# Performance work log

Hardware: AMD Instinct MI355X
Metric: run time of the kernel (lower is better)

Reference implementation:

```python
import jax, jax.numpy as jnp
import numpy as np

N_NODES = 245760      # 8192 graphs * 30 atoms
N_GRAPHS = 8192
N_EDGES = 1000000
NODES_PER_GRAPH = 30
F_NODE = 78
F_CELL = 1000
HID = 64


def _lin(key, fan_in, fan_out):
    kw, kb = jax.random.split(key)
    s = 1.0 / np.sqrt(fan_in)
    W = jax.random.uniform(kw, (fan_in, fan_out), minval=-s, maxval=s, dtype=jnp.float32)
    b = jax.random.uniform(kb, (fan_out,), minval=-s, maxval=s, dtype=jnp.float32)
    return W, b


def setup_inputs() -> dict:
    key = jax.random.key(0)
    ks = jax.random.split(key, 14)
    x = jax.random.normal(ks[0], (N_NODES, F_NODE), dtype=jnp.float32)
    # edges constrained within each graph: node = graph_id * 30 + local offset
    offs = jax.random.randint(ks[1], (2, N_EDGES), 0, NODES_PER_GRAPH)
    ge = jax.random.randint(ks[2], (N_EDGES,), 0, N_GRAPHS)
    edge_index = (ge[None, :] * NODES_PER_GRAPH + offs).astype(jnp.int64)
    batch = jnp.repeat(jnp.arange(N_GRAPHS, dtype=jnp.int64), NODES_PER_GRAPH)
    cell_features = jax.random.normal(ks[3], (N_GRAPHS, F_CELL), dtype=jnp.float32)
    W1, b1 = _lin(ks[4], F_NODE, HID)
    W2, b2 = _lin(ks[5], HID, 2 * HID)
    W3, b3 = _lin(ks[6], 2 * HID, 4 * HID)
    Wd, bd = _lin(ks[7], 4 * HID, HID)          # drug_embed_fc
    Wc1, bc1 = _lin(ks[8], F_CELL, 2 * HID)      # cell_fc1
    Wc2, bc2 = _lin(ks[9], 2 * HID, HID)         # cell_fc2
    Wm1, bm1 = _lin(ks[10], 2 * HID, HID)        # combiner_fc1
    Wm2, bm2 = _lin(ks[11], HID, 32)             # combiner_fc2
    Wo, bo = _lin(ks[12], 32, 1)                 # output_fc
    return {"x": x, "edge_index": edge_index, "batch": batch,
            "cell_features": cell_features,
            "W1": W1, "b1": b1, "W2": W2, "b2": b2, "W3": W3, "b3": b3,
            "Wd": Wd, "bd": bd, "Wc1": Wc1, "bc1": bc1, "Wc2": Wc2, "bc2": bc2,
            "Wm1": Wm1, "bm1": bm1, "Wm2": Wm2, "bm2": bm2, "Wo": Wo, "bo": bo}


def _gcn_conv(h, W, b, srcA, dstA, norm, n_nodes):
    # PyG GCNConv: linear transform, then sym-normalized scatter-add (self-loops included in srcA/dstA/norm)
    h = h @ W                                   # [N, out]
    msg = h[srcA] * norm[:, None]               # gather + edge scaling
    out = jnp.zeros((n_nodes, W.shape[1]), h.dtype).at[dstA].add(msg)
    return out + b


def reference(x, edge_index, batch, cell_features,
              W1, b1, W2, b2, W3, b3, Wd, bd,
              Wc1, bc1, Wc2, bc2, Wm1, bm1, Wm2, bm2, Wo, bo):
    n = x.shape[0]
    loops = jnp.arange(n, dtype=edge_index.dtype)
    srcA = jnp.concatenate([edge_index[0], loops])
    dstA = jnp.concatenate([edge_index[1], loops])
    deg = jax.ops.segment_sum(jnp.ones_like(dstA, dtype=x.dtype), dstA, num_segments=n)
    dinv = jax.lax.rsqrt(deg)                   # deg >= 1 due to self-loops
    norm = dinv[srcA] * dinv[dstA]

    h = jax.nn.relu(_gcn_conv(x, W1, b1, srcA, dstA, norm, n))
    h = jax.nn.relu(_gcn_conv(h, W2, b2, srcA, dstA, norm, n))
    h = jax.nn.relu(_gcn_conv(h, W3, b3, srcA, dstA, norm, n))

    # global mean pool over graphs
    sums = jax.ops.segment_sum(h, batch, num_segments=N_GRAPHS)
    cnts = jax.ops.segment_sum(jnp.ones((n,), h.dtype), batch, num_segments=N_GRAPHS)
    drug = (sums / cnts[:, None]) @ Wd + bd     # [B, HID]

    cell = jax.nn.relu(cell_features @ Wc1 + bc1)
    cell = cell @ Wc2 + bc2                      # [B, HID]

    comb = jnp.concatenate([drug, cell], axis=1)
    z = jax.nn.relu(comb @ Wm1 + bm1)
    z = jax.nn.relu(z @ Wm2 + bm2)
    out = z @ Wo + bo
    return out.reshape(-1)
```

## Files before the change

kernel.cpp:

```cpp
#include <hip/hip_runtime.h>

typedef __attribute__((ext_vector_type(8))) short short8;
typedef __attribute__((ext_vector_type(4))) short short4v;
typedef __attribute__((ext_vector_type(4))) float f32x4;
typedef unsigned short u16;

__device__ __forceinline__ u16 f2bf(float f) {
    union { float f; unsigned u; } v; v.f = f;
    unsigned r = v.u + 0x7FFFu + ((v.u >> 16) & 1u);
    return (u16)(r >> 16);
}
__device__ __forceinline__ float bf2f(u16 h) {
    union { unsigned u; float f; } v; v.u = ((unsigned)h) << 16;
    return v.f;
}
__device__ __forceinline__ void split2(float f, u16& h, u16& l) {
    h = f2bf(f);
    l = f2bf(f - bf2f(h));
}
__device__ __forceinline__ short8 ld8(const u16* p) {
    short4v a = *(const short4v*)p;
    short4v b = *(const short4v*)(p + 4);
    short8 r;
    r[0] = a[0]; r[1] = a[1]; r[2] = a[2]; r[3] = a[3];
    r[4] = b[0]; r[5] = b[1]; r[6] = b[2]; r[7] = b[3];
    return r;
}
#define MFMA(A, B, C) __builtin_amdgcn_mfma_f32_16x16x32_bf16(A, B, C, 0, 0, 0)


__global__ void k_zero4(int4* __restrict__ p, int n4) {
    int i = blockIdx.x * 256 + threadIdx.x;
    if (i < n4) p[i] = make_int4(0, 0, 0, 0);
}

__global__ void k_cnt(const int* __restrict__ ei, unsigned* __restrict__ A32, int E) {
    int e = blockIdx.x * 256 + threadIdx.x;
    if (e >= E) return;
    int s = ei[e], d = ei[E + e];
    int g = d / 30;
    int idx = g * 960 + (d - g * 30) * 32 + (s - g * 30);
    atomicAdd(&A32[idx >> 1], 1u << ((idx & 1) * 16));
}

__global__ void k_split_t(const float* __restrict__ W, u16* __restrict__ th,
                          u16* __restrict__ tl, int K, int F, int Kp) {
    int idx = blockIdx.x * 256 + threadIdx.x;
    if (idx >= F * Kp) return;
    int f = idx / Kp, k = idx % Kp;
    float v = (k < K) ? W[(size_t)k * F + f] : 0.f;
    u16 h, l; split2(v, h, l);
    th[idx] = h; tl[idx] = l;
}

__global__ __launch_bounds__(512, 8) void k_node(
    const float* __restrict__ x, const unsigned* __restrict__ A32,
    const u16* __restrict__ W1h, const u16* __restrict__ W1l,
    const u16* __restrict__ W2h, const u16* __restrict__ W2l,
    const u16* __restrict__ W3h, const u16* __restrict__ W3l,
    const float* __restrict__ b1, const float* __restrict__ b2,
    const float* __restrict__ b3, float* __restrict__ P) {
    __shared__ __align__(16) char smem[39936];
    u16* xh  = (u16*)(smem + 0);
    u16* xl  = (u16*)(smem + 6400);
    u16* h1h = (u16*)(smem + 0);
    u16* h1l = (u16*)(smem + 4352);
    u16* a3h = (u16*)(smem + 0);
    u16* a3l = (u16*)(smem + 8448);
    float* Afp = (float*)(smem + 16896);
    float* dv  = (float*)(smem + 20736);
    u16* t1h = (u16*)(smem + 16896);
    u16* t1l = (u16*)(smem + 21504);
    u16* h2h = (u16*)(smem + 16896);
    u16* h2l = (u16*)(smem + 26112);
    u16* Ah  = (u16*)(smem + 35328);
    u16* Al  = (u16*)(smem + 37632);

    int t = threadIdx.x;
    int g = blockIdx.x;
    int wave = t >> 6, lane = t & 63, quad = lane >> 4, l15 = lane & 15;

    {
        for (int i = t; i < 860; i += 512) {
            uint* arr = (uint*)((i >= 430) ? (char*)xl : (char*)xh);
            int j = (i >= 430) ? i - 430 : i;
            int r, c32;
            if (j < 330) { r = j / 11; c32 = 39 + j % 11; }
            else { r = 30 + (j - 330) / 50; c32 = (j - 330) % 50; }
            arr[r * 50 + c32] = 0;
        }
        const float4* xg = (const float4*)(x + (size_t)g * 2340);
        for (int i = t; i < 585; i += 512) {
            float4 v = xg[i];
            int base = i * 4;
            float vv[4] = {v.x, v.y, v.z, v.w};
#pragma unroll
            for (int j = 0; j < 4; j++) {
                int idx = base + j;
                int r = idx / 78, c = idx - r * 78;
                u16 h, l; split2(vv[j], h, l);
                xh[r * 100 + c] = h; xl[r * 100 + c] = l;
            }
        }
        const unsigned* ac = A32 + (size_t)g * 480;
        for (int i = t; i < 480; i += 512) {
            unsigned w = ac[i];
            Afp[2 * i] = (float)(w & 0xFFFFu);
            Afp[2 * i + 1] = (float)(w >> 16);
        }
        if (t < 32) {
            float s = 1.f;
            if (t < 30) {
                const unsigned* rp = ac + t * 16;
                unsigned acc = 0;
#pragma unroll
                for (int j = 0; j < 16; j++) { unsigned w = rp[j]; acc += (w & 0xFFFFu) + (w >> 16); }
                s += (float)acc;
            }
            dv[t] = (t < 30) ? rsqrtf(s) : 0.f;
        }
    }
    __syncthreads();
    {
#pragma unroll
        for (int ii = 0; ii < 2; ii++) {
            int i = t + ii * 512;
            int r = i >> 5, c = i & 31;
            float a = 0.f;
            if (r < 30 && c < 30)
                a = (Afp[r * 32 + c] + (r == c ? 1.f : 0.f)) * dv[r] * dv[c];
            u16 h, l; split2(a, h, l);
            Ah[r * 36 + c] = h; Al[r * 36 + c] = l;
        }
    }
    __syncthreads();
    {
        int wm = wave >> 2, wn = wave & 3;
        int arow = wm * 16 + l15;
        int col = wn * 16 + l15;
        const u16* wph = W1h + col * 96 + quad * 8;
        const u16* wpl = W1l + col * 96 + quad * 8;
        f32x4 acc = {0.f, 0.f, 0.f, 0.f};
#pragma unroll
        for (int ch = 0; ch < 3; ch++) {
            int kc = ch * 32;
            short8 bh = *(const short8*)(wph + kc);
            short8 bl = *(const short8*)(wpl + kc);
            short8 ah = ld8(&xh[arow * 100 + kc + quad * 8]);
            short8 al = ld8(&xl[arow * 100 + kc + quad * 8]);
            acc = MFMA(ah, bh, acc);
            acc = MFMA(al, bh, acc);
            acc = MFMA(ah, bl, acc);
        }
#pragma unroll
        for (int rg = 0; rg < 4; rg++) {
            int row = wm * 16 + quad * 4 + rg;
            u16 h, l; split2(acc[rg], h, l);
            t1h[col * 36 + row] = h;
            t1l[col * 36 + row] = l;
        }
    }
    __syncthreads();
    {
        int wm = wave >> 2, wn = wave & 3;
        int arow = wm * 16 + l15;
        int col = wn * 16 + l15;
        short8 aAh = ld8(&Ah[arow * 36 + quad * 8]);
        short8 aAl = ld8(&Al[arow * 36 + quad * 8]);
        short8 bh = ld8(&t1h[col * 36 + quad * 8]);
        short8 bl = ld8(&t1l[col * 36 + quad * 8]);
        f32x4 acc = {0.f, 0.f, 0.f, 0.f};
        acc = MFMA(aAh, bh, acc);
        acc = MFMA(aAl, bh, acc);
        acc = MFMA(aAh, bl, acc);
        float bb = b1[col];
#pragma unroll
        for (int rg = 0; rg < 4; rg++) {
            int row = wm * 16 + quad * 4 + rg;
            float v = fmaxf(acc[rg] + bb, 0.f);
            u16 h, l; split2(v, h, l);
            h1h[row * 68 + col] = h;
            h1l[row * 68 + col] = l;
        }
    }
    __syncthreads();
    {
        int col = wave * 16 + l15;
        const u16* wph = W2h + col * 64 + quad * 8;
        const u16* wpl = W2l + col * 64 + quad * 8;
        f32x4 acc[2] = {{0.f,0.f,0.f,0.f},{0.f,0.f,0.f,0.f}};
#pragma unroll
        for (int ch = 0; ch < 2; ch++) {
            int kc = ch * 32;
            short8 bh = *(const short8*)(wph + kc);
            short8 bl = *(const short8*)(wpl + kc);
#pragma unroll
            for (int mi = 0; mi < 2; mi++) {
                short8 ah = ld8(&h1h[(mi * 16 + l15) * 68 + kc + quad * 8]);
                short8 al = ld8(&h1l[(mi * 16 + l15) * 68 + kc + quad * 8]);
                acc[mi] = MFMA(ah, bh, acc[mi]);
                acc[mi] = MFMA(al, bh, acc[mi]);
                acc[mi] = MFMA(ah, bl, acc[mi]);
            }
        }
        float bb = b2[col];
#pragma unroll
        for (int mi = 0; mi < 2; mi++)
#pragma unroll
            for (int rg = 0; rg < 4; rg++) {
                int row = mi * 16 + quad * 4 + rg;
                float v = fmaxf(acc[mi][rg] + bb, 0.f);
                u16 h, l; split2(v, h, l);
                h2h[col * 36 + row] = h;
                h2l[col * 36 + row] = l;
            }
    }
    __syncthreads();
    {
        int col = wave * 16 + l15;
        short8 bh = ld8(&h2h[col * 36 + quad * 8]);
        short8 bl = ld8(&h2l[col * 36 + quad * 8]);
        f32x4 acc[2] = {{0.f,0.f,0.f,0.f},{0.f,0.f,0.f,0.f}};
#pragma unroll
        for (int mi = 0; mi < 2; mi++) {
            short8 aAh = ld8(&Ah[(mi * 16 + l15) * 36 + quad * 8]);
            short8 aAl = ld8(&Al[(mi * 16 + l15) * 36 + quad * 8]);
            acc[mi] = MFMA(aAh, bh, acc[mi]);
            acc[mi] = MFMA(aAl, bh, acc[mi]);
            acc[mi] = MFMA(aAh, bl, acc[mi]);
        }
#pragma unroll
        for (int mi = 0; mi < 2; mi++)
#pragma unroll
            for (int rg = 0; rg < 4; rg++) {
                int row = mi * 16 + quad * 4 + rg;
                u16 h, l; split2(acc[mi][rg], h, l);
                a3h[row * 132 + col] = h;
                a3l[row * 132 + col] = l;
            }
    }
    __syncthreads();
    {
        int colb = wave * 32;
        f32x4 acc[2][2] = {{{0.f,0.f,0.f,0.f},{0.f,0.f,0.f,0.f}},
                           {{0.f,0.f,0.f,0.f},{0.f,0.f,0.f,0.f}}};
        short8 cwh[2], cwl[2], nwh[2], nwl[2];
#pragma unroll
        for (int ni = 0; ni < 2; ni++) {
            size_t o = (size_t)(colb + ni * 16 + l15) * 128 + quad * 8;
            cwh[ni] = *(const short8*)(W3h + o);
            cwl[ni] = *(const short8*)(W3l + o);
        }
#pragma unroll
        for (int ch = 0; ch < 4; ch++) {
            if (ch < 3) {
#pragma unroll
                for (int ni = 0; ni < 2; ni++) {
                    size_t o = (size_t)(colb + ni * 16 + l15) * 128 + (ch + 1) * 32 + quad * 8;
                    nwh[ni] = *(const short8*)(W3h + o);
                    nwl[ni] = *(const short8*)(W3l + o);
                }
            }
            short8 ah[2], al[2];
#pragma unroll
            for (int mi = 0; mi < 2; mi++) {
                ah[mi] = ld8(&a3h[(mi * 16 + l15) * 132 + ch * 32 + quad * 8]);
                al[mi] = ld8(&a3l[(mi * 16 + l15) * 132 + ch * 32 + quad * 8]);
            }
#pragma unroll
            for (int mi = 0; mi < 2; mi++)
#pragma unroll
                for (int ni = 0; ni < 2; ni++) {
                    acc[mi][ni] = MFMA(ah[mi], cwh[ni], acc[mi][ni]);
                    acc[mi][ni] = MFMA(al[mi], cwh[ni], acc[mi][ni]);
                    acc[mi][ni] = MFMA(ah[mi], cwl[ni], acc[mi][ni]);
                }
            if (ch < 3) {
#pragma unroll
                for (int ni = 0; ni < 2; ni++) { cwh[ni] = nwh[ni]; cwl[ni] = nwl[ni]; }
            }
        }
#pragma unroll
        for (int ni = 0; ni < 2; ni++) {
            int col = colb + ni * 16 + l15;
            float bb = b3[col];
            float p = 0.f;
#pragma unroll
            for (int mi = 0; mi < 2; mi++)
#pragma unroll
                for (int rg = 0; rg < 4; rg++) {
                    int row = mi * 16 + quad * 4 + rg;
                    if (row < 30) p += fmaxf(acc[mi][ni][rg] + bb, 0.f);
                }
            p += __shfl_down(p, 32);
            p += __shfl_down(p, 16);
            if (lane < 16)
                P[(size_t)g * 256 + colb + ni * 16 + lane] = p * (1.0f / 30.0f);
        }
    }
}

__global__ __launch_bounds__(256) void k_cell(const float* __restrict__ cf,
        const u16* __restrict__ Wth, const u16* __restrict__ Wtl,
        const float* __restrict__ bias, float* __restrict__ Y) {
    __shared__ __align__(16) u16 Xh[32 * 140];
    __shared__ __align__(16) u16 Xl[32 * 140];
    int t = threadIdx.x;
    int row0 = blockIdx.x * 32;
    int wave = t >> 6, lane = t & 63, quad = lane >> 4, l15 = lane & 15;
    f32x4 acc[2][2] = {{{0.f,0.f,0.f,0.f},{0.f,0.f,0.f,0.f}},
                       {{0.f,0.f,0.f,0.f},{0.f,0.f,0.f,0.f}}};
    for (int ko = 0; ko < 8; ko++) {
#pragma unroll
        for (int ii = 0; ii < 4; ii++) {
            int i = t + ii * 256;
            int r = i >> 5, c4 = i & 31;
            int col = ko * 128 + c4 * 4;
            float4 v = {0.f, 0.f, 0.f, 0.f};
            if (col < 1000) v = *(const float4*)(cf + (size_t)(row0 + r) * 1000 + col);
            float vv[4] = {v.x, v.y, v.z, v.w};
#pragma unroll
            for (int j = 0; j < 4; j++) {
                u16 h, l; split2(vv[j], h, l);
                Xh[r * 140 + c4 * 4 + j] = h;
                Xl[r * 140 + c4 * 4 + j] = l;
            }
        }
        __syncthreads();
#pragma unroll
        for (int kk = 0; kk < 4; kk++) {
            int klo = kk * 32 + quad * 8;
            short8 ah[2], al[2];
#pragma unroll
            for (int mi = 0; mi < 2; mi++) {
                ah[mi] = ld8(&Xh[(mi * 16 + l15) * 140 + klo]);
                al[mi] = ld8(&Xl[(mi * 16 + l15) * 140 + klo]);
            }
#pragma unroll
            for (int ni = 0; ni < 2; ni++) {
                int col = wave * 32 + ni * 16 + l15;
                size_t o = (size_t)col * 1024 + ko * 128 + kk * 32 + quad * 8;
                short8 bh = *(const short8*)(Wth + o);
                short8 bl = *(const short8*)(Wtl + o);
#pragma unroll
                for (int mi = 0; mi < 2; mi++) {
                    acc[mi][ni] = MFMA(ah[mi], bh, acc[mi][ni]);
                    acc[mi][ni] = MFMA(al[mi], bh, acc[mi][ni]);
                    acc[mi][ni] = MFMA(ah[mi], bl, acc[mi][ni]);
                }
            }
        }
        __syncthreads();
    }
#pragma unroll
    for (int ni = 0; ni < 2; ni++) {
        int col = wave * 32 + ni * 16 + l15;
        float bv = bias[col];
#pragma unroll
        for (int mi = 0; mi < 2; mi++)
#pragma unroll
            for (int rg = 0; rg < 4; rg++) {
                int row = row0 + mi * 16 + quad * 4 + rg;
                Y[(size_t)row * 128 + col] = fmaxf(acc[mi][ni][rg] + bv, 0.f);
            }
    }
}

__global__ __launch_bounds__(256) void k_tail(const float* __restrict__ pooled,
        const float* __restrict__ cell1,
        const float* __restrict__ Wd, const float* __restrict__ bd,
        const float* __restrict__ Wc2, const float* __restrict__ bc2,
        const float* __restrict__ Wm1, const float* __restrict__ bm1,
        const float* __restrict__ Wm2, const float* __restrict__ bm2,
        const float* __restrict__ Wo, const float* __restrict__ bo,
        float* __restrict__ out) {
    __shared__ float pr[1024];
    __shared__ float c1[512];
    __shared__ float dz[512];
    __shared__ float z1f[256];
    __shared__ float z2f[128];
    int t = threadIdx.x;
    int g0 = blockIdx.x * 4;
    int gl = t >> 6, c = t & 63;
    ((float4*)pr)[t] = ((const float4*)(pooled + (size_t)g0 * 256))[t];
    if (t < 128) ((float4*)c1)[t] = ((const float4*)(cell1 + (size_t)g0 * 128))[t];
    __syncthreads();
    float s = bd[c];
#pragma unroll 8
    for (int k = 0; k < 256; k++) s += pr[gl * 256 + k] * Wd[k * 64 + c];
    dz[gl * 128 + c] = s;
    float s2 = bc2[c];
#pragma unroll 8
    for (int k = 0; k < 128; k++) s2 += c1[gl * 128 + k] * Wc2[k * 64 + c];
    dz[gl * 128 + 64 + c] = s2;
    __syncthreads();
    float s3 = bm1[c];
#pragma unroll 8
    for (int k = 0; k < 128; k++) s3 += dz[gl * 128 + k] * Wm1[k * 64 + c];
    z1f[gl * 64 + c] = fmaxf(s3, 0.f);
    __syncthreads();
    if (c < 32) {
        float s4 = bm2[c];
#pragma unroll 8
        for (int k = 0; k < 64; k++) s4 += z1f[gl * 64 + k] * Wm2[k * 32 + c];
        z2f[gl * 32 + c] = fmaxf(s4, 0.f);
    }
    __syncthreads();
    float v = (c < 32) ? z2f[gl * 32 + c] * Wo[c] : 0.f;
#pragma unroll
    for (int off = 32; off > 0; off >>= 1) v += __shfl_down(v, off);
    if (c == 0) out[g0 + gl] = v + bo[0];
}


extern "C" void kernel_launch(void* const* d_in, const int* in_sizes, int n_in,
                              void* d_out, int out_size, void* d_ws, size_t ws_size,
                              hipStream_t stream) {
    const float* x   = (const float*)d_in[0];
    const int*   ei  = (const int*)d_in[1];
    const float* cf  = (const float*)d_in[3];
    const float* W1  = (const float*)d_in[4];
    const float* b1  = (const float*)d_in[5];
    const float* W2  = (const float*)d_in[6];
    const float* b2  = (const float*)d_in[7];
    const float* W3  = (const float*)d_in[8];
    const float* b3  = (const float*)d_in[9];
    const float* Wd  = (const float*)d_in[10];
    const float* bd  = (const float*)d_in[11];
    const float* Wc1 = (const float*)d_in[12];
    const float* bc1 = (const float*)d_in[13];
    const float* Wc2 = (const float*)d_in[14];
    const float* bc2 = (const float*)d_in[15];
    const float* Wm1 = (const float*)d_in[16];
    const float* bm1 = (const float*)d_in[17];
    const float* Wm2 = (const float*)d_in[18];
    const float* bm2 = (const float*)d_in[19];
    const float* Wo  = (const float*)d_in[20];
    const float* bo  = (const float*)d_in[21];
    float* out = (float*)d_out;

    const int E = in_sizes[1] / 2;
    const int B = in_sizes[3] / 1000;

    char* w = (char*)d_ws;
    auto carve = [&](size_t bytes) { void* p = (void*)w; w += (bytes + 255) & ~(size_t)255; return p; };
    unsigned* A32 = (unsigned*)carve((size_t)B * 960 * 2);
    float* pooled = (float*)carve((size_t)B * 256 * 4);
    float* cell1  = (float*)carve((size_t)B * 128 * 4);
    u16* W1th = (u16*)carve(64 * 96 * 2);     u16* W1tl = (u16*)carve(64 * 96 * 2);
    u16* W2th = (u16*)carve(128 * 64 * 2);    u16* W2tl = (u16*)carve(128 * 64 * 2);
    u16* W3th = (u16*)carve(256 * 128 * 2);   u16* W3tl = (u16*)carve(256 * 128 * 2);
    u16* Wc1th = (u16*)carve(128 * 1024 * 2); u16* Wc1tl = (u16*)carve(128 * 1024 * 2);

    auto g1 = [](int n) { return (n + 255) / 256; };

    k_zero4<<<g1(B * 120), 256, 0, stream>>>((int4*)A32, B * 120);
    k_cnt<<<g1(E), 256, 0, stream>>>(ei, A32, E);

    k_split_t<<<g1(64 * 96), 256, 0, stream>>>(W1, W1th, W1tl, 78, 64, 96);
    k_split_t<<<g1(128 * 64), 256, 0, stream>>>(W2, W2th, W2tl, 64, 128, 64);
    k_split_t<<<g1(256 * 128), 256, 0, stream>>>(W3, W3th, W3tl, 128, 256, 128);
    k_split_t<<<g1(128 * 1024), 256, 0, stream>>>(Wc1, Wc1th, Wc1tl, 1000, 128, 1024);

    k_node<<<B, 512, 0, stream>>>(x, A32,
                                  W1th, W1tl, W2th, W2tl, W3th, W3tl,
                                  b1, b2, b3, pooled);

    k_cell<<<B / 32, 256, 0, stream>>>(cf, Wc1th, Wc1tl, bc1, cell1);

    k_tail<<<B / 4, 256, 0, stream>>>(pooled, cell1, Wd, bd, Wc2, bc2,
                                      Wm1, bm1, Wm2, bm2, Wo, bo, out);
}
```

Before: 473.6 us.

## Merge prep kernels and fold cell MLP blocks into node kernel launch

The zeroing and four weight-split launches are merged into one prep kernel. The cell_fc1 GEMM now runs as extra leading blocks of the node kernel, 64 rows per 512-thread block, so it executes alongside the per-graph GCN blocks instead of as a separate launch. The cell tile staging now writes packed short4 vectors to shared memory instead of scalar stores. This cuts launch count and the tail of the cell kernel, at the cost of some branch divergence and register pressure shared between two code paths in one kernel.

New measurement: 445.8 us. -5.9%, faster.

```diff
diff --git a/kernel.cpp b/kernel.cpp
--- a/kernel.cpp
+++ b/kernel.cpp
@@ -28,10 +28,24 @@
 }
 #define MFMA(A, B, C) __builtin_amdgcn_mfma_f32_16x16x32_bf16(A, B, C, 0, 0, 0)
 
-
-__global__ void k_zero4(int4* __restrict__ p, int n4) {
+__global__ __launch_bounds__(256) void k_prep(int4* __restrict__ A32z, int nz4,
+        const float* __restrict__ W1, u16* __restrict__ W1h, u16* __restrict__ W1l,
+        const float* __restrict__ W2, u16* __restrict__ W2h, u16* __restrict__ W2l,
+        const float* __restrict__ W3, u16* __restrict__ W3h, u16* __restrict__ W3l,
+        const float* __restrict__ Wc1, u16* __restrict__ Wc1h, u16* __restrict__ Wc1l) {
     int i = blockIdx.x * 256 + threadIdx.x;
-    if (i < n4) p[i] = make_int4(0, 0, 0, 0);
+    if (i < nz4) { A32z[i] = make_int4(0, 0, 0, 0); return; }
+    i -= nz4;
+    const float* W; u16 *th, *tl; int K, F, Kp;
+    if (i < 6144)                        { W = W1;  th = W1h;  tl = W1l;  K = 78;   F = 64;  Kp = 96; }
+    else if (i < 6144 + 8192)            { i -= 6144; W = W2;  th = W2h;  tl = W2l;  K = 64;   F = 128; Kp = 64; }
+    else if (i < 6144 + 8192 + 32768)    { i -= 6144 + 8192; W = W3;  th = W3h;  tl = W3l;  K = 128;  F = 256; Kp = 128; }
+    else if (i < 6144 + 8192 + 32768 + 131072) { i -= 6144 + 8192 + 32768; W = Wc1; th = Wc1h; tl = Wc1l; K = 1000; F = 128; Kp = 1024; }
+    else return;
+    int f = i / Kp, k = i - f * Kp;
+    float v = (k < K) ? W[(size_t)k * F + f] : 0.f;
+    u16 h, l; split2(v, h, l);
+    th[i] = h; tl[i] = l;
 }
 
 __global__ void k_cnt(const int* __restrict__ ei, unsigned* __restrict__ A32, int E) {
@@ -43,24 +57,88 @@
     atomicAdd(&A32[idx >> 1], 1u << ((idx & 1) * 16));
 }
 
-__global__ void k_split_t(const float* __restrict__ W, u16* __restrict__ th,
-                          u16* __restrict__ tl, int K, int F, int Kp) {
-    int idx = blockIdx.x * 256 + threadIdx.x;
-    if (idx >= F * Kp) return;
-    int f = idx / Kp, k = idx % Kp;
-    float v = (k < K) ? W[(size_t)k * F + f] : 0.f;
-    u16 h, l; split2(v, h, l);
-    th[idx] = h; tl[idx] = l;
-}
-
-__global__ __launch_bounds__(512, 8) void k_node(
+__global__ __launch_bounds__(512, 8) void k_nodecell(
     const float* __restrict__ x, const unsigned* __restrict__ A32,
     const u16* __restrict__ W1h, const u16* __restrict__ W1l,
     const u16* __restrict__ W2h, const u16* __restrict__ W2l,
     const u16* __restrict__ W3h, const u16* __restrict__ W3l,
     const float* __restrict__ b1, const float* __restrict__ b2,
-    const float* __restrict__ b3, float* __restrict__ P) {
+    const float* __restrict__ b3, float* __restrict__ P,
+    const float* __restrict__ cf,
+    const u16* __restrict__ Wc1h, const u16* __restrict__ Wc1l,
+    const float* __restrict__ bc1, float* __restrict__ cell1,
+    int CELLB) {
     __shared__ __align__(16) char smem[39936];
+    int t = threadIdx.x;
+    int wave = t >> 6, lane = t & 63, quad = lane >> 4, l15 = lane & 15;
+
+    if (blockIdx.x < CELLB) {
+        u16* Xh = (u16*)(smem + 0);
+        u16* Xl = (u16*)(smem + 17920);
+        int row0 = blockIdx.x * 64;
+        int half = wave >> 2, wq = wave & 3;
+        f32x4 acc[2][2] = {{{0.f,0.f,0.f,0.f},{0.f,0.f,0.f,0.f}},
+                           {{0.f,0.f,0.f,0.f},{0.f,0.f,0.f,0.f}}};
+        for (int ko = 0; ko < 8; ko++) {
+#pragma unroll
+            for (int ii = 0; ii < 4; ii++) {
+                int i = t + ii * 512;
+                int r = i >> 5, c4 = i & 31;
+                int col = ko * 128 + c4 * 4;
+                float4 v = {0.f, 0.f, 0.f, 0.f};
+                if (col < 1000) v = *(const float4*)(cf + (size_t)(row0 + r) * 1000 + col);
+                float vv[4] = {v.x, v.y, v.z, v.w};
+                short4v hs, ls;
+#pragma unroll
+                for (int j = 0; j < 4; j++) {
+                    u16 h, l; split2(vv[j], h, l);
+                    hs[j] = (short)h; ls[j] = (short)l;
+                }
+                *(short4v*)(Xh + r * 140 + c4 * 4) = hs;
+                *(short4v*)(Xl + r * 140 + c4 * 4) = ls;
+            }
+            __syncthreads();
+#pragma unroll
+            for (int kk = 0; kk < 4; kk++) {
+                int klo = kk * 32 + quad * 8;
+                short8 ah[2], al[2];
+#pragma unroll
+                for (int mi = 0; mi < 2; mi++) {
+                    ah[mi] = ld8(&Xh[(half * 32 + mi * 16 + l15) * 140 + klo]);
+                    al[mi] = ld8(&Xl[(half * 32 + mi * 16 + l15) * 140 + klo]);
+                }
+#pragma unroll
+                for (int ni = 0; ni < 2; ni++) {
+                    int col = wq * 32 + ni * 16 + l15;
+                    size_t o = (size_t)col * 1024 + ko * 128 + kk * 32 + quad * 8;
+                    short8 bh = *(const short8*)(Wc1h + o);
+                    short8 bl = *(const short8*)(Wc1l + o);
+#pragma unroll
+                    for (int mi = 0; mi < 2; mi++) {
+                        acc[mi][ni] = MFMA(ah[mi], bh, acc[mi][ni]);
+                        acc[mi][ni] = MFMA(al[mi], bh, acc[mi][ni]);
+                        acc[mi][ni] = MFMA(ah[mi], bl, acc[mi][ni]);
+                    }
+                }
+            }
+            __syncthreads();
+        }
+#pragma unroll
+        for (int ni = 0; ni < 2; ni++) {
+            int col = wq * 32 + ni * 16 + l15;
+            float bv = bc1[col];
+#pragma unroll
+            for (int mi = 0; mi < 2; mi++)
+#pragma unroll
+                for (int rg = 0; rg < 4; rg++) {
+                    int row = row0 + half * 32 + mi * 16 + quad * 4 + rg;
+                    cell1[(size_t)row * 128 + col] = fmaxf(acc[mi][ni][rg] + bv, 0.f);
+                }
+        }
+        return;
+    }
+
+    int g = blockIdx.x - CELLB;
     u16* xh  = (u16*)(smem + 0);
     u16* xl  = (u16*)(smem + 6400);
     u16* h1h = (u16*)(smem + 0);
@@ -76,10 +154,6 @@
     u16* Ah  = (u16*)(smem + 35328);
     u16* Al  = (u16*)(smem + 37632);
 
-    int t = threadIdx.x;
-    int g = blockIdx.x;
-    int wave = t >> 6, lane = t & 63, quad = lane >> 4, l15 = lane & 15;
-
     {
         for (int i = t; i < 860; i += 512) {
             uint* arr = (uint*)((i >= 430) ? (char*)xl : (char*)xh);
@@ -297,72 +371,6 @@
             if (lane < 16)
                 P[(size_t)g * 256 + colb + ni * 16 + lane] = p * (1.0f / 30.0f);
         }
-    }
-}
-
-__global__ __launch_bounds__(256) void k_cell(const float* __restrict__ cf,
-        const u16* __restrict__ Wth, const u16* __restrict__ Wtl,
-        const float* __restrict__ bias, float* __restrict__ Y) {
-    __shared__ __align__(16) u16 Xh[32 * 140];
-    __shared__ __align__(16) u16 Xl[32 * 140];
-    int t = threadIdx.x;
-    int row0 = blockIdx.x * 32;
-    int wave = t >> 6, lane = t & 63, quad = lane >> 4, l15 = lane & 15;
-    f32x4 acc[2][2] = {{{0.f,0.f,0.f,0.f},{0.f,0.f,0.f,0.f}},
-                       {{0.f,0.f,0.f,0.f},{0.f,0.f,0.f,0.f}}};
-    for (int ko = 0; ko < 8; ko++) {
-#pragma unroll
-        for (int ii = 0; ii < 4; ii++) {
-            int i = t + ii * 256;
-            int r = i >> 5, c4 = i & 31;
-            int col = ko * 128 + c4 * 4;
-            float4 v = {0.f, 0.f, 0.f, 0.f};
-            if (col < 1000) v = *(const float4*)(cf + (size_t)(row0 + r) * 1000 + col);
-            float vv[4] = {v.x, v.y, v.z, v.w};
-#pragma unroll
-            for (int j = 0; j < 4; j++) {
-                u16 h, l; split2(vv[j], h, l);
-                Xh[r * 140 + c4 * 4 + j] = h;
-                Xl[r * 140 + c4 * 4 + j] = l;
-            }
-        }
-        __syncthreads();
-#pragma unroll
-        for (int kk = 0; kk < 4; kk++) {
-            int klo = kk * 32 + quad * 8;
-            short8 ah[2], al[2];
-#pragma unroll
-            for (int mi = 0; mi < 2; mi++) {
-                ah[mi] = ld8(&Xh[(mi * 16 + l15) * 140 + klo]);
-                al[mi] = ld8(&Xl[(mi * 16 + l15) * 140 + klo]);
-            }
-#pragma unroll
-            for (int ni = 0; ni < 2; ni++) {
-                int col = wave * 32 + ni * 16 + l15;
-                size_t o = (size_t)col * 1024 + ko * 128 + kk * 32 + quad * 8;
-                short8 bh = *(const short8*)(Wth + o);
-                short8 bl = *(const short8*)(Wtl + o);
-#pragma unroll
-                for (int mi = 0; mi < 2; mi++) {
-                    acc[mi][ni] = MFMA(ah[mi], bh, acc[mi][ni]);
-                    acc[mi][ni] = MFMA(al[mi], bh, acc[mi][ni]);
-                    acc[mi][ni] = MFMA(ah[mi], bl, acc[mi][ni]);
-                }
-            }
-        }
-        __syncthreads();
-    }
-#pragma unroll
-    for (int ni = 0; ni < 2; ni++) {
-        int col = wave * 32 + ni * 16 + l15;
-        float bv = bias[col];
-#pragma unroll
-        for (int mi = 0; mi < 2; mi++)
-#pragma unroll
-            for (int rg = 0; rg < 4; rg++) {
-                int row = row0 + mi * 16 + quad * 4 + rg;
-                Y[(size_t)row * 128 + col] = fmaxf(acc[mi][ni][rg] + bv, 0.f);
-            }
     }
 }
 
@@ -454,19 +462,19 @@
 
     auto g1 = [](int n) { return (n + 255) / 256; };
 
-    k_zero4<<<g1(B * 120), 256, 0, stream>>>((int4*)A32, B * 120);
+    const int nz4 = B * 120;
+    const int nsplit = 6144 + 8192 + 32768 + 131072;
+
+    k_prep<<<g1(nz4 + nsplit), 256, 0, stream>>>((int4*)A32, nz4,
+        W1, W1th, W1tl, W2, W2th, W2tl, W3, W3th, W3tl, Wc1, Wc1th, Wc1tl);
+
     k_cnt<<<g1(E), 256, 0, stream>>>(ei, A32, E);
 
-    k_split_t<<<g1(64 * 96), 256, 0, stream>>>(W1, W1th, W1tl, 78, 64, 96);
-    k_split_t<<<g1(128 * 64), 256, 0, stream>>>(W2, W2th, W2tl, 64, 128, 64);
-    k_split_t<<<g1(256 * 128), 256, 0, stream>>>(W3, W3th, W3tl, 128, 256, 128);
-    k_split_t<<<g1(128 * 1024), 256, 0, stream>>>(Wc1, Wc1th, Wc1tl, 1000, 128, 1024);
-
-    k_node<<<B, 512, 0, stream>>>(x, A32,
+    const int CELLB = B / 64;
+    k_nodecell<<<CELLB + B, 512, 0, stream>>>(x, A32,
                                   W1th, W1tl, W2th, W2tl, W3th, W3tl,
-                                  b1, b2, b3, pooled);
-
-    k_cell<<<B / 32, 256, 0, stream>>>(cf, Wc1th, Wc1tl, bc1, cell1);
+                                  b1, b2, b3, pooled,
+                                  cf, Wc1th, Wc1tl, bc1, cell1, CELLB);
 
     k_tail<<<B / 4, 256, 0, stream>>>(pooled, cell1, Wd, bd, Wc2, bc2,
                                       Wm1, bm1, Wm2, bm2, Wo, bo, out);
```
